# Performance work log

Hardware: AMD Instinct MI355X
Metric: run time of the kernel (lower is better)

The kernel has to match this reference:

```python
import jax, jax.numpy as jnp
import numpy as np

B, S, E, H = 2, 2048, 1024, 16
HD = E // H
SCALE = 1.0 / np.sqrt(HD)
PR_QKV = 0.05   # precision_ratio for q/k/v (critical_attention=False)
PR_OUT = 0.10
ROUTE_THR = 0.05  # gradient_threshold (critical_attention=False)
LN_EPS = 1e-5


def rpb_linear(x, W, b, precision_ratio):
    """ResidualPrecisionBoostLinear: ternary-quantized weight (threshold 0.7*mean|W|,
    per-tensor scale) plus top-`precision_ratio` fraction of residual kept full precision."""
    absW = jnp.abs(W)
    thr = 0.7 * jnp.mean(absW)
    tmask = (absW > thr).astype(W.dtype)
    scale = jnp.sum(absW * tmask) / jnp.maximum(jnp.sum(tmask), 1.0)
    Wq = scale * jnp.sign(W) * tmask
    res = W - Wq
    k = int(precision_ratio * W.size)
    kth = jax.lax.top_k(jnp.abs(res).ravel(), k)[0][-1]
    W_eff = Wq + res * (jnp.abs(res) >= kth).astype(W.dtype)
    return x @ W_eff.T + b


def selective_route(x, threshold):
    # forward: zero out small-magnitude activations (straight-through in training)
    return x * (jnp.abs(x) >= threshold).astype(x.dtype)


def layer_norm(x, g, b):
    mu = jnp.mean(x, axis=-1, keepdims=True)
    var = jnp.mean(jnp.square(x - mu), axis=-1, keepdims=True)
    return (x - mu) * jax.lax.rsqrt(var + LN_EPS) * g + b


def setup_inputs() -> dict:
    key = jax.random.key(0)
    ks = jax.random.split(key, 12)
    f = lambda k, shp, s=1.0: jax.random.normal(k, shp, dtype=jnp.float32) * s
    return {
        "query": f(ks[0], (B, S, E)),
        "key": f(ks[1], (B, S, E)),
        "value": f(ks[2], (B, S, E)),
        "Wq": f(ks[3], (E, E), 0.02), "bq": jnp.zeros((E,), jnp.float32),
        "Wk": f(ks[4], (E, E), 0.02), "bk": jnp.zeros((E,), jnp.float32),
        "Wv": f(ks[5], (E, E), 0.02), "bv": jnp.zeros((E,), jnp.float32),
        "Wo": f(ks[6], (E, E), 0.02), "bo": jnp.zeros((E,), jnp.float32),
        "ln_g": jnp.ones((E,), jnp.float32),
        "ln_b": jnp.zeros((E,), jnp.float32),
    }


def reference(query, key, value, Wq, bq, Wk, bk, Wv, bv, Wo, bo, ln_g, ln_b):
    qn = layer_norm(query, ln_g, ln_b)
    q = selective_route(rpb_linear(qn, Wq, bq, PR_QKV), ROUTE_THR)
    k = selective_route(rpb_linear(key, Wk, bk, PR_QKV), ROUTE_THR)
    v = selective_route(rpb_linear(value, Wv, bv, PR_QKV), ROUTE_THR)
    # [B,S,E] -> [B,H,S,HD]
    q = q.reshape(B, S, H, HD).transpose(0, 2, 1, 3)
    k = k.reshape(B, S, H, HD).transpose(0, 2, 1, 3)
    v = v.reshape(B, S, H, HD).transpose(0, 2, 1, 3)
    scores = jnp.einsum("bhqd,bhkd->bhqk", q, k) * SCALE
    attn = jax.nn.softmax(scores, axis=-1)   # dropout is identity in eval
    ctx = jnp.einsum("bhqk,bhkd->bhqd", attn, v)
    ctx = ctx.transpose(0, 2, 1, 3).reshape(B, S, E)
    return rpb_linear(ctx, Wo, bo, PR_OUT)
```

## Files before the change

### kernel.cpp

```cpp
#include <hip/hip_runtime.h>
#include <stdio.h>
#include <stdint.h>

#define BB 2
#define SS 2048
#define ED 1024
#define HH 16
#define HDD 64
#define MROWS 4096
#define NW_ELEM 1048576u

typedef unsigned short ushortT;
typedef __attribute__((ext_vector_type(8))) short bf16x8;
typedef __attribute__((ext_vector_type(4))) float f32x4;
typedef __attribute__((ext_vector_type(16))) float f32x16;

#define U_WHI 0u
#define U_WLO 4194304u
#define U_XQ  8388608u
#define U_XK  12582912u
#define U_XV  16777216u
#define U_QH  20971520u
#define U_KH  25165824u
#define U_VH  29360128u
#define LP_OFF  33554432u
#define P0_OFF  67108864u
#define P1_OFF  83886080u
#define SMALL_OFF  100663296u
#define HIST_OFF   SMALL_OFF
#define ABS_OFF    (SMALL_OFF + 16384u)
#define MSK_OFF    (ABS_OFF + 32u)
#define CNT_OFF    (MSK_OFF + 32u)
#define SMALL_BYTES 16464u
#define WS_NEEDED  (SMALL_OFF + SMALL_BYTES)

#define SC44 17592186044416.0f
#define INV44 (1.0 / 17592186044416.0)
#define QSCALE 0.18033688011112042f

__device__ __forceinline__ const float* wsel(int w, const float* W0, const float* W1,
                                             const float* W2, const float* W3) {
  return w == 0 ? W0 : w == 1 ? W1 : w == 2 ? W2 : W3;
}

__device__ __forceinline__ ushortT f2bf(float x) {
  unsigned u = __float_as_uint(x);
  unsigned r = (u + 0x7FFFu + ((u >> 16) & 1u)) >> 16;
  return (ushortT)r;
}
__device__ __forceinline__ float bf2f(ushortT b) {
  return __uint_as_float(((unsigned)b) << 16);
}
__device__ __forceinline__ void bsplit(float x, ushortT& h, ushortT& l) {
  ushortT hb = f2bf(x);
  float hf = bf2f(hb);
  h = hb;
  l = f2bf(x - hf);
}
__device__ __forceinline__ unsigned pkbf(float a, float b) {
  unsigned r;
  asm("v_cvt_pk_bf16_f32 %0, %1, %2" : "=v"(r) : "v"(a), "v"(b));
  return r;
}
__device__ __forceinline__ void plswap(unsigned& a, unsigned& b) {
  asm("v_permlane32_swap_b32 %0, %1" : "+v"(a), "+v"(b));
}
__device__ __forceinline__ float fexp2(float x) {
#if __has_builtin(__builtin_amdgcn_exp2f)
  return __builtin_amdgcn_exp2f(x);
#else
  float r;
  asm("v_exp_f32 %0, %1\n\ts_nop 1" : "=v"(r) : "v"(x));
  return r;
#endif
}

__device__ __forceinline__ void gld_lds16(const ushortT* g, ushortT* s) {
  __builtin_amdgcn_global_load_lds((__attribute__((address_space(1))) void*)g,
                                   (__attribute__((address_space(3))) void*)s, 16, 0, 0);
}

template <int N> __device__ __forceinline__ void waitv() {
  if constexpr (N == 0) asm volatile("s_waitcnt vmcnt(0)" ::: "memory");
  else if constexpr (N == 4) asm volatile("s_waitcnt vmcnt(4)" ::: "memory");
  else if constexpr (N == 6) asm volatile("s_waitcnt vmcnt(6)" ::: "memory");
}
__device__ __forceinline__ void pipe_barrier() {
  __builtin_amdgcn_s_barrier();
  __builtin_amdgcn_sched_barrier(0);
}

__device__ __forceinline__ float get_thr(const unsigned long long* sAbs, int w) {
  return 0.7f * (float)((double)sAbs[w] * INV44 / 1048576.0);
}
__device__ __forceinline__ float get_scale(const unsigned long long* sMsk,
                                           const unsigned* cnt, int w) {
  double s = (double)sMsk[w] * INV44;
  return (float)s / fmaxf((float)cnt[w], 1.0f);
}

__device__ __forceinline__ void scan_sel(const unsigned* hist, unsigned& k, unsigned& prefix,
                                         unsigned* sh, int t) {
  sh[t] = hist[t];
  __syncthreads();
  for (int off = 1; off < 256; off <<= 1) {
    unsigned add = (t + off < 256) ? sh[t + off] : 0u;
    __syncthreads();
    sh[t] += add;
    __syncthreads();
  }
  int sel = __syncthreads_count((int)(sh[t] >= k)) - 1;
  unsigned suf = sh[sel];
  k -= (suf - hist[sel]);
  prefix = (prefix << 8) | (unsigned)sel;
  __syncthreads();
}

__global__ __launch_bounds__(256) void k_wstats(const float* W0, const float* W1,
                                                const float* W2, const float* W3,
                                                unsigned long long* sAbs) {
  const int w = blockIdx.y, t = threadIdx.x;
  const float* W = wsel(w, W0, W1, W2, W3) + blockIdx.x * 4096;
  unsigned long long s = 0;
#pragma unroll
  for (int r = 0; r < 4; r++) {
    float4 v = *(const float4*)(W + (t + 256 * r) * 4);
    s += (unsigned long long)(fabsf(v.x) * SC44);
    s += (unsigned long long)(fabsf(v.y) * SC44);
    s += (unsigned long long)(fabsf(v.z) * SC44);
    s += (unsigned long long)(fabsf(v.w) * SC44);
  }
  __shared__ unsigned long long sd[256];
  sd[t] = s;
  __syncthreads();
  for (int off = 128; off > 0; off >>= 1) {
    if (t < off) sd[t] += sd[t + off];
    __syncthreads();
  }
  if (!t) atomicAdd(&sAbs[w], sd[0]);
}

__global__ __launch_bounds__(256) void k_masked(const float* W0, const float* W1,
                                                const float* W2, const float* W3,
                                                const unsigned long long* sAbs,
                                                unsigned long long* sMsk, unsigned* sCnt) {
  const int w = blockIdx.y, t = threadIdx.x;
  const float thr = get_thr(sAbs, w);
  const float* W = wsel(w, W0, W1, W2, W3) + blockIdx.x * 4096;
  unsigned long long s = 0;
  unsigned c = 0;
#pragma unroll
  for (int r = 0; r < 4; r++) {
    float4 v = *(const float4*)(W + (t + 256 * r) * 4);
    float xs[4] = {v.x, v.y, v.z, v.w};
#pragma unroll
    for (int q = 0; q < 4; q++) {
      float a = fabsf(xs[q]);
      if (a > thr) { s += (unsigned long long)(a * SC44); c++; }
    }
  }
  __shared__ unsigned long long sd[256];
  __shared__ unsigned sc[256];
  sd[t] = s; sc[t] = c;
  __syncthreads();
  for (int off = 128; off > 0; off >>= 1) {
    if (t < off) { sd[t] += sd[t + off]; sc[t] += sc[t + off]; }
    __syncthreads();
  }
  if (!t) { atomicAdd(&sMsk[w], sd[0]); atomicAdd(&sCnt[w], sc[0]); }
}

__global__ __launch_bounds__(256) void k_hist(const float* W0, const float* W1,
                                              const float* W2, const float* W3,
                                              const unsigned long long* sAbs,
                                              const unsigned long long* sMsk,
                                              const unsigned* sCnt,
                                              unsigned* histG, int pass) {
  const int w = blockIdx.y, t = threadIdx.x;
  __shared__ unsigned sh[256];
  __shared__ unsigned h[256];
  const float thr = get_thr(sAbs, w);
  const float scale = get_scale(sMsk, sCnt, w);
  unsigned k = (w == 3) ? 104857u : 52428u, prefix = 0u;
  for (int pp = 0; pp < pass; pp++)
    scan_sel(histG + (pp * 4 + w) * 256, k, prefix, sh, t);

  h[t] = 0;
  __syncthreads();
  const float* W = wsel(w, W0, W1, W2, W3) + blockIdx.x * 4096;
  const int shift1 = 32 - 8 * pass;
  const int shift2 = 24 - 8 * pass;
#pragma unroll
  for (int r = 0; r < 4; r++) {
    float4 v = *(const float4*)(W + (t + 256 * r) * 4);
    float xs[4] = {v.x, v.y, v.z, v.w};
#pragma unroll
    for (int q = 0; q < 4; q++) {
      float x = xs[q];
      float a = fabsf(x);
      float wq = (a > thr) ? copysignf(scale, x) : 0.0f;
      unsigned bits = __float_as_uint(fabsf(x - wq));
      if (pass == 0) {
        atomicAdd(&h[bits >> 24], 1u);
      } else {
        if ((bits >> shift1) == prefix)
          atomicAdd(&h[(bits >> shift2) & 255u], 1u);
      }
    }
  }
  __syncthreads();
  if (h[t]) atomicAdd(&histG[(pass * 4 + w) * 256 + t], h[t]);
}

__global__ __launch_bounds__(256) void k_weff(const float* W0, const float* W1,
                                              const float* W2, const float* W3,
                                              const unsigned long long* sAbs,
                                              const unsigned long long* sMsk,
                                              const unsigned* sCnt,
                                              const unsigned* histG,
                                              ushortT* Whi, ushortT* Wlo) {
  const int w = blockIdx.y, t = threadIdx.x;
  __shared__ unsigned sh[256];
  const float thr = get_thr(sAbs, w);
  const float scale = get_scale(sMsk, sCnt, w);
  unsigned k = (w == 3) ? 104857u : 52428u, kth = 0u;
  for (int pp = 0; pp < 4; pp++)
    scan_sel(histG + (pp * 4 + w) * 256, k, kth, sh, t);

  const unsigned idx = (blockIdx.x * 256 + t) * 4;
  const float* W = wsel(w, W0, W1, W2, W3);
  float4 v = *(const float4*)(W + idx);
  float xs[4] = {v.x, v.y, v.z, v.w};
  ushort4 h4, l4;
#pragma unroll
  for (int c = 0; c < 4; c++) {
    float x = xs[c];
    float a = fabsf(x);
    float wq = (a > thr) ? copysignf(scale, x) : 0.0f;
    float res = x - wq;
    unsigned bits = __float_as_uint(fabsf(res));
    float we = wq + ((bits >= kth) ? res : 0.0f);
    ushortT hh, ll;
    bsplit(we, hh, ll);
    ((ushortT*)&h4)[c] = hh;
    ((ushortT*)&l4)[c] = ll;
  }
  *(ushort4*)&Whi[(size_t)w * NW_ELEM + idx] = h4;
  *(ushort4*)&Wlo[(size_t)w * NW_ELEM + idx] = l4;
}

__global__ __launch_bounds__(256) void k_pre(const float* __restrict__ query,
                                             const float* __restrict__ key,
                                             const float* __restrict__ value,
                                             const float* __restrict__ g,
                                             const float* __restrict__ b,
                                             ushortT* __restrict__ Xq,
                                             ushortT* __restrict__ Xk,
                                             ushortT* __restrict__ Xv) {
  const int t = threadIdx.x;
  if (blockIdx.y == 0) {
    const int row = blockIdx.x;
    __shared__ float red[8];
    float4 v = *(const float4*)&query[(size_t)row * ED + t * 4];
    float s = v.x + v.y + v.z + v.w;
#pragma unroll
    for (int m = 32; m; m >>= 1) s += __shfl_xor(s, m, 64);
    if ((t & 63) == 0) red[t >> 6] = s;
    __syncthreads();
    float mu = (red[0] + red[1] + red[2] + red[3]) * (1.0f / 1024.0f);
    float dx = v.x - mu, dy = v.y - mu, dz = v.z - mu, dw = v.w - mu;
    float s2 = dx * dx + dy * dy + dz * dz + dw * dw;
#pragma unroll
    for (int m = 32; m; m >>= 1) s2 += __shfl_xor(s2, m, 64);
    if ((t & 63) == 0) red[4 + (t >> 6)] = s2;
    __syncthreads();
    float var = (red[4] + red[5] + red[6] + red[7]) * (1.0f / 1024.0f);
    float inv = rsqrtf(var + 1e-5f);
    float4 gg = *(const float4*)&g[t * 4];
    float4 bb = *(const float4*)&b[t * 4];
    float ys[4] = {dx * inv * gg.x + bb.x, dy * inv * gg.y + bb.y,
                   dz * inv * gg.z + bb.z, dw * inv * gg.w + bb.w};
    ushort4 h4;
#pragma unroll
    for (int c = 0; c < 4; c++) ((ushortT*)&h4)[c] = f2bf(ys[c]);
    *(ushort4*)&Xq[(size_t)row * ED + t * 4] = h4;
  } else {
    const float* src = (blockIdx.y == 1) ? key : value;
    ushortT* dst = (blockIdx.y == 1) ? Xk : Xv;
    const int i = (blockIdx.x * 256 + t) * 4;
    float4 v = *(const float4*)&src[i];
    ushort4 h4;
    h4.x = f2bf(v.x); h4.y = f2bf(v.y); h4.z = f2bf(v.z); h4.w = f2bf(v.w);
    *(ushort4*)&dst[i] = h4;
  }
}

__device__ __forceinline__ f32x4 mfma16(bf16x8 a, bf16x8 b, f32x4 c) {
  return __builtin_amdgcn_mfma_f32_16x16x32_bf16(a, b, c, 0, 0, 0);
}

template <int MODE, bool ALO, bool WLO, int BK, int MINW>
__global__ __launch_bounds__(256, MINW) void k_gemmP(
    const ushortT* __restrict__ A0, const ushortT* __restrict__ A0l,
    const ushortT* __restrict__ A1,
    const ushortT* __restrict__ Wh, const ushortT* __restrict__ Wl,
    const float* __restrict__ bias0, const float* __restrict__ bias1,
    ushortT* __restrict__ Cb0, ushortT* __restrict__ Cb1,
    float* __restrict__ Cf) {
  constexpr int ABUF = (BK == 64) ? 8192 : 4096;
  constexpr int BBUF = (BK == 64) ? 4096 : 2048;
  constexpr int L = ((BK == 64) ? 4 : 2) * (1 + (ALO ? 1 : 0)) +
                    ((BK == 64) ? 2 : 1) * (1 + (WLO ? 1 : 0));
  constexpr int NT = 1024 / BK;
  __shared__ __align__(16) ushortT sAh[3 * ABUF];
  __shared__ __align__(16) ushortT sAl[ALO ? 3 * ABUF : 8];
  __shared__ __align__(16) ushortT sBh[3 * BBUF];
  __shared__ __align__(16) ushortT sBl[WLO ? 3 * BBUF : 8];

  const int t = threadIdx.x;
  const int w = t >> 6, l = t & 63;
  const int wr = w >> 1, wc = w & 1;

  const int which = (MODE == 0) ? (blockIdx.x >> 9) : 0;
  const int wid = blockIdx.x & 511;
  int id2 = (wid & 7) * 64 + (wid >> 3);
  const int m0 = (id2 >> 4) * 128, n0 = (id2 & 15) * 64;

  const ushortT* A = (MODE == 0 && which) ? A1 : A0;
  const ushortT* Wha = Wh + (MODE == 0 ? (unsigned)which * NW_ELEM : 0u);
  const float* bias = (MODE == 0 && which) ? bias1 : bias0;

  const int sr = l >> 3, swz = (l & 7) ^ sr;
  const int srow = l >> 2, sgr = (l & 3) ^ ((l >> 3) & 3);

  auto stage = [&](int kt, int buf) {
    if constexpr (BK == 64) {
#pragma unroll
      for (int s2 = 0; s2 < 4; s2++) {
        int seg = w * 4 + s2;
        size_t ga = (size_t)(m0 + seg * 8 + sr) * ED + kt * 64 + swz * 8;
        gld_lds16(A + ga, sAh + buf * ABUF + seg * 512);
        if constexpr (ALO) gld_lds16(A0l + ga, sAl + buf * ABUF + seg * 512);
      }
#pragma unroll
      for (int s2 = 0; s2 < 2; s2++) {
        int seg = w * 2 + s2;
        size_t gb = (size_t)(n0 + seg * 8 + sr) * ED + kt * 64 + swz * 8;
        gld_lds16(Wha + gb, sBh + buf * BBUF + seg * 512);
        if constexpr (WLO) gld_lds16(Wl + gb, sBl + buf * BBUF + seg * 512);
      }
    } else {
#pragma unroll
      for (int s2 = 0; s2 < 2; s2++) {
        int seg = w * 2 + s2;
        size_t ga = (size_t)(m0 + seg * 16 + srow) * ED + kt * 32 + sgr * 8;
        gld_lds16(A + ga, sAh + buf * ABUF + seg * 512);
        if constexpr (ALO) gld_lds16(A0l + ga, sAl + buf * ABUF + seg * 512);
      }
      {
        size_t gb = (size_t)(n0 + w * 16 + srow) * ED + kt * 32 + sgr * 8;
        gld_lds16(Wha + gb, sBh + buf * BBUF + w * 512);
        if constexpr (WLO) gld_lds16(Wl + gb, sBl + buf * BBUF + w * 512);
      }
    }
  };

  f32x4 acc[4][2];
#pragma unroll
  for (int i = 0; i < 4; i++)
#pragma unroll
    for (int j = 0; j < 2; j++) acc[i][j] = (f32x4){0.0f, 0.0f, 0.0f, 0.0f};

  auto compute = [&](int buf) {
    if constexpr (BK == 64) {
#pragma unroll
      for (int ks = 0; ks < 2; ks++) {
        bf16x8 ah[4], al[4], bh2[2], bl2[2];
        const int G = ks * 4 + (l >> 4);
#pragma unroll
        for (int i = 0; i < 4; i++) {
          int r = wr * 64 + i * 16 + (l & 15);
          int off = buf * ABUF + r * 64 + ((G ^ (l & 7)) << 3);
          ah[i] = *(const bf16x8*)&sAh[off];
          if constexpr (ALO) al[i] = *(const bf16x8*)&sAl[off];
        }
#pragma unroll
        for (int j = 0; j < 2; j++) {
          int r = wc * 32 + j * 16 + (l & 15);
          int off = buf * BBUF + r * 64 + ((G ^ (l & 7)) << 3);
          bh2[j] = *(const bf16x8*)&sBh[off];
          if constexpr (WLO) bl2[j] = *(const bf16x8*)&sBl[off];
        }
#pragma unroll
        for (int i = 0; i < 4; i++)
#pragma unroll
          for (int j = 0; j < 2; j++) {
            acc[i][j] = mfma16(ah[i], bh2[j], acc[i][j]);
            if constexpr (WLO) acc[i][j] = mfma16(ah[i], bl2[j], acc[i][j]);
            if constexpr (ALO) acc[i][j] = mfma16(al[i], bh2[j], acc[i][j]);
          }
      }
    } else {
      bf16x8 ah[4], al[4], bh2[2], bl2[2];
      const int G = l >> 4;
#pragma unroll
      for (int i = 0; i < 4; i++) {
        int r = wr * 64 + i * 16 + (l & 15);
        int off = buf * ABUF + r * 32 + ((G ^ ((r >> 1) & 3)) << 3);
        ah[i] = *(const bf16x8*)&sAh[off];
        if constexpr (ALO) al[i] = *(const bf16x8*)&sAl[off];
      }
#pragma unroll
      for (int j = 0; j < 2; j++) {
        int r = wc * 32 + j * 16 + (l & 15);
        int off = buf * BBUF + r * 32 + ((G ^ ((r >> 1) & 3)) << 3);
        bh2[j] = *(const bf16x8*)&sBh[off];
        if constexpr (WLO) bl2[j] = *(const bf16x8*)&sBl[off];
      }
#pragma unroll
      for (int i = 0; i < 4; i++)
#pragma unroll
        for (int j = 0; j < 2; j++) {
          acc[i][j] = mfma16(ah[i], bh2[j], acc[i][j]);
          if constexpr (WLO) acc[i][j] = mfma16(ah[i], bl2[j], acc[i][j]);
          if constexpr (ALO) acc[i][j] = mfma16(al[i], bh2[j], acc[i][j]);
        }
    }
  };

  stage(0, 0);
  stage(1, 1);
  for (int kt = 0; kt < NT; ++kt) {
    if (kt < NT - 1) waitv<L>(); else waitv<0>();
    pipe_barrier();
    if (kt + 2 < NT) stage(kt + 2, (kt + 2) % 3);
    __builtin_amdgcn_s_setprio(1);
    compute(kt % 3);
    __builtin_amdgcn_s_setprio(0);
  }

  const int coln = l & 15, row4 = (l >> 4) * 4;
  float bn[2];
#pragma unroll
  for (int j = 0; j < 2; j++) bn[j] = bias[n0 + wc * 32 + j * 16 + coln];
  const int b_ = m0 >> 11, h_ = n0 >> 6;

  if constexpr (MODE == 1) {
#pragma unroll
    for (int i = 0; i < 4; i++)
#pragma unroll
      for (int j = 0; j < 2; j++) {
        int n = n0 + wc * 32 + j * 16 + coln;
#pragma unroll
        for (int r = 0; r < 4; r++) {
          int m = m0 + wr * 64 + i * 16 + row4 + r;
          Cf[(size_t)m * ED + n] = acc[i][j][r] + bn[j];
        }
      }
  } else if constexpr (MODE == 0) {
    const float osc = (which == 0) ? QSCALE : 1.0f;
    ushortT* C = which ? Cb1 : Cb0;
#pragma unroll
    for (int i = 0; i < 4; i++)
#pragma unroll
      for (int j = 0; j < 2; j++) {
        int hd = wc * 32 + j * 16 + coln;
#pragma unroll
        for (int r = 0; r < 4; r++) {
          int m = m0 + wr * 64 + i * 16 + row4 + r;
          int s_ = m & 2047;
          float y = acc[i][j][r] + bn[j];
          y = (fabsf(y) >= 0.05f) ? y : 0.0f;
          y *= osc;
          C[((size_t)(b_ * HH + h_) * SS + s_) * HDD + hd] = f2bf(y);
        }
      }
  } else {
#pragma unroll
    for (int i = 0; i < 4; i++)
#pragma unroll
      for (int j = 0; j < 2; j++) {
        int hd = wc * 32 + j * 16 + coln;
        int s0_ = (m0 + wr * 64 + i * 16 + row4) & 2047;
        ushort4 h4;
#pragma unroll
        for (int r = 0; r < 4; r++) {
          float y = acc[i][j][r] + bn[j];
          y = (fabsf(y) >= 0.05f) ? y : 0.0f;
          ((ushortT*)&h4)[r] = f2bf(y);
        }
        *(ushort4*)&Cb0[((size_t)(b_ * HH + h_) * HDD + hd) * SS + s0_] = h4;
      }
  }
}

__device__ __forceinline__ f32x16 mfma32(bf16x8 a, bf16x8 b, f32x16 c) {
  return __builtin_amdgcn_mfma_f32_32x32x16_bf16(a, b, c, 0, 0, 0);
}

__device__ __forceinline__ void exppack(const f32x16& A, float* ls4,
                                        bf16x8& paA, bf16x8& paB) {
  float p[16];
#pragma unroll
  for (int r = 0; r < 16; r++) {
    p[r] = fexp2(A[r]);
    ls4[r & 3] += p[r];
  }
  unsigned c0 = pkbf(p[0], p[1]), c1 = pkbf(p[2], p[3]);
  unsigned c2 = pkbf(p[4], p[5]), c3 = pkbf(p[6], p[7]);
  unsigned c4 = pkbf(p[8], p[9]), c5 = pkbf(p[10], p[11]);
  unsigned c6 = pkbf(p[12], p[13]), c7 = pkbf(p[14], p[15]);
  plswap(c0, c2); plswap(c1, c3); plswap(c4, c6); plswap(c5, c7);
  uint4 ta = make_uint4(c0, c1, c2, c3);
  uint4 tb = make_uint4(c4, c5, c6, c7);
  paA = __builtin_bit_cast(bf16x8, ta);
  paB = __builtin_bit_cast(bf16x8, tb);
}

__global__ __launch_bounds__(256, 4) void k_attn(
    const ushortT* __restrict__ Qh, const ushortT* __restrict__ Kh,
    const ushortT* __restrict__ Vh,
    float* __restrict__ Pp, float* __restrict__ Lp) {
  __shared__ __align__(16) ushortT sK[2 * 4096];
  __shared__ __align__(16) ushortT sV[2 * 4096];

  const int t = threadIdx.x;
  const int w = t >> 6, l = t & 63;
  const int l32 = l & 31, g = l >> 5;

  int id = blockIdx.x;
  int id2 = (id & 7) * 128 + (id >> 3);
  const int bh = id2 >> 5;
  const int qt = (id2 >> 1) & 15;
  const int half = id2 & 1;

  const size_t kqbase = (size_t)bh * (SS * HDD);
  const size_t vbase = (size_t)bh * (HDD * SS);
  const int q0 = qt * 128 + w * 32;
  const int sbase = half * 1024;

  bf16x8 qh[4];
  const size_t qrow = kqbase + (size_t)(q0 + l32) * HDD;
#pragma unroll
  for (int ks = 0; ks < 4; ks++) qh[ks] = *(const bf16x8*)&Qh[qrow + ks * 16 + g * 8];

  f32x16 octx0, octx1;
#pragma unroll
  for (int i = 0; i < 16; i++) { octx0[i] = 0.0f; octx1[i] = 0.0f; }
  float ls4[4] = {0.0f, 0.0f, 0.0f, 0.0f};

  const int srow = l >> 3;
  const int sgr = (l & 7) ^ srow;

  auto stageA = [&](int kt, int buf) {
    const int s0 = sbase + kt * 64;
#pragma unroll
    for (int s2 = 0; s2 < 2; s2++) {
      int seg = w * 2 + s2;
      int row = seg * 8 + srow;
      gld_lds16(Kh + kqbase + (size_t)(s0 + row) * HDD + sgr * 8, sK + buf * 4096 + seg * 512);
      gld_lds16(Vh + vbase + (size_t)row * SS + s0 + sgr * 8, sV + buf * 4096 + seg * 512);
    }
  };

  stageA(0, 0);
  __syncthreads();

  for (int kt = 0; kt < 16; ++kt) {
    if (kt < 15) stageA(kt + 1, (kt + 1) & 1);
    const ushortT* cK = sK + (kt & 1) * 4096;
    const ushortT* cV = sV + (kt & 1) * 4096;

    f32x16 acc0, acc1;
#pragma unroll
    for (int i = 0; i < 16; i++) { acc0[i] = 0.0f; acc1[i] = 0.0f; }
#pragma unroll
    for (int ks = 0; ks < 4; ks++) {
      int sw = ((ks * 2 + g) ^ (l32 & 7)) << 3;
      bf16x8 kh0 = *(const bf16x8*)&cK[l32 * 64 + sw];
      bf16x8 kh1 = *(const bf16x8*)&cK[(32 + l32) * 64 + sw];
      acc0 = mfma32(kh0, qh[ks], acc0);
      acc1 = mfma32(kh1, qh[ks], acc1);
    }

    bf16x8 pa0, pa1, pa2, pa3;
    exppack(acc0, ls4, pa0, pa1);
    exppack(acc1, ls4, pa2, pa3);

#pragma unroll
    for (int js = 0; js < 4; js++) {
      bf16x8 pj = js == 0 ? pa0 : js == 1 ? pa1 : js == 2 ? pa2 : pa3;
      int vsw = ((js * 2 + g) ^ (l32 & 7)) << 3;
      bf16x8 vh0 = *(const bf16x8*)&cV[l32 * 64 + vsw];
      bf16x8 vh1 = *(const bf16x8*)&cV[(32 + l32) * 64 + vsw];
      octx0 = mfma32(pj, vh0, octx0);
      octx1 = mfma32(pj, vh1, octx1);
    }
    __syncthreads();
  }

  float lsum = (ls4[0] + ls4[1]) + (ls4[2] + ls4[3]);
  float ls = lsum + __shfl_xor(lsum, 32, 64);
  if (g == 0) Lp[half * 65536 + bh * 2048 + q0 + l32] = ls;

  float* P = Pp + (size_t)half * 4194304u;
#pragma unroll
  for (int r = 0; r < 16; r++) {
    int q = (r & 3) + 8 * (r >> 2) + 4 * g;
    size_t pb = ((size_t)bh * 2048 + q0 + q) * 64;
    P[pb + l32] = octx0[r];
    P[pb + 32 + l32] = octx1[r];
  }
}

__global__ __launch_bounds__(256) void k_reduce(const float* __restrict__ Pp,
                                                const float* __restrict__ Lp,
                                                ushortT* __restrict__ ctxH,
                                                ushortT* __restrict__ ctxL) {
  const unsigned i4 = (blockIdx.x * 256 + threadIdx.x) * 4;
  const int d = i4 & 63;
  const int sq = (i4 >> 6) & 2047;
  const int bh = i4 >> 17;
  float ls = Lp[bh * 2048 + sq] + Lp[65536 + bh * 2048 + sq];
  float inv = 1.0f / ls;
  float4 a = *(const float4*)&Pp[i4];
  float4 b = *(const float4*)&Pp[4194304u + i4];
  float os[4] = {(a.x + b.x) * inv, (a.y + b.y) * inv,
                 (a.z + b.z) * inv, (a.w + b.w) * inv};
  ushort4 h4, l4;
#pragma unroll
  for (int c = 0; c < 4; c++) {
    ushortT hh, ll;
    bsplit(os[c], hh, ll);
    ((ushortT*)&h4)[c] = hh;
    ((ushortT*)&l4)[c] = ll;
  }
  size_t ci = ((size_t)((bh >> 4) * 2048 + sq)) * 1024 + (bh & 15) * 64 + d;
  *(ushort4*)&ctxH[ci] = h4;
  *(ushort4*)&ctxL[ci] = l4;
}

extern "C" void kernel_launch(void* const* d_in, const int* in_sizes, int n_in,
                              void* d_out, int out_size, void* d_ws, size_t ws_size,
                              hipStream_t stream) {
  const float* query = (const float*)d_in[0];
  const float* key   = (const float*)d_in[1];
  const float* value = (const float*)d_in[2];
  const float* Wq = (const float*)d_in[3];
  const float* bq = (const float*)d_in[4];
  const float* Wk = (const float*)d_in[5];
  const float* bk = (const float*)d_in[6];
  const float* Wv = (const float*)d_in[7];
  const float* bv = (const float*)d_in[8];
  const float* Wo = (const float*)d_in[9];
  const float* bo = (const float*)d_in[10];
  const float* lng = (const float*)d_in[11];
  const float* lnb = (const float*)d_in[12];
  float* out = (float*)d_out;

  if (ws_size < (size_t)WS_NEEDED) {
    fprintf(stderr, "kernel_launch: ws too small (%zu < %u)\n", ws_size, WS_NEEDED);
    return;
  }

  ushortT* wsu = (ushortT*)d_ws;
  ushortT* Whi = wsu + U_WHI;
  ushortT* Wlo = wsu + U_WLO;
  ushortT* Xq  = wsu + U_XQ;
  ushortT* Xk  = wsu + U_XK;
  ushortT* Xv  = wsu + U_XV;
  ushortT* Qhp = wsu + U_QH;
  ushortT* Khp = wsu + U_KH;
  ushortT* Vhp = wsu + U_VH;
  ushortT* Chp = wsu + U_XQ;
  ushortT* Clp = wsu + U_XK;

  char* wsb = (char*)d_ws;
  float* Pp = (float*)(wsb + P0_OFF);
  float* Lp = (float*)(wsb + LP_OFF);
  unsigned* histG = (unsigned*)(wsb + HIST_OFF);
  unsigned long long* sAbs = (unsigned long long*)(wsb + ABS_OFF);
  unsigned long long* sMsk = (unsigned long long*)(wsb + MSK_OFF);
  unsigned* sCnt = (unsigned*)(wsb + CNT_OFF);

  hipMemsetAsync(histG, 0, SMALL_BYTES, stream);

  k_pre<<<dim3(MROWS, 3), 256, 0, stream>>>(query, key, value, lng, lnb, Xq, Xk, Xv);

  dim3 gW(256, 4);
  k_wstats<<<gW, 256, 0, stream>>>(Wq, Wk, Wv, Wo, sAbs);
  k_masked<<<gW, 256, 0, stream>>>(Wq, Wk, Wv, Wo, sAbs, sMsk, sCnt);
  for (int pass = 0; pass < 4; ++pass)
    k_hist<<<gW, 256, 0, stream>>>(Wq, Wk, Wv, Wo, sAbs, sMsk, sCnt, histG, pass);
  k_weff<<<dim3(1024, 4), 256, 0, stream>>>(Wq, Wk, Wv, Wo, sAbs, sMsk, sCnt, histG,
                                            Whi, Wlo);

  k_gemmP<0, false, false, 64, 2><<<1024, 256, 0, stream>>>(
      Xq, nullptr, Xk, Whi, nullptr, bq, bk, Qhp, Khp, nullptr);
  k_gemmP<2, false, true, 32, 3><<<512, 256, 0, stream>>>(
      Xv, nullptr, nullptr, Whi + 2 * NW_ELEM, Wlo + 2 * NW_ELEM, bv, nullptr,
      Vhp, nullptr, nullptr);

  k_attn<<<1024, 256, 0, stream>>>(Qhp, Khp, Vhp, Pp, Lp);
  k_reduce<<<4096, 256, 0, stream>>>(Pp, Lp, Chp, Clp);

  k_gemmP<1, true, true, 32, 2><<<512, 256, 0, stream>>>(
      Chp, Clp, nullptr, Whi + 3 * NW_ELEM, Wlo + 3 * NW_ELEM, bo, nullptr,
      nullptr, nullptr, out);
}
```

Before: 241.7 us.

## Fuse preprocessing and weight-quantization kernels into one cooperative persistent kernel

Replaces the memset, the LN/cast kernel, and the eight weight-statistics, histogram-radix-select and W_eff kernels with a single cooperative launch of 512 blocks. Grid-wide syncs separate the phases, and the histogram and counter zeroing moves inside the kernel. This removes per-launch overhead and launch gaps across roughly ten small kernels. In exchange, the fixed 512-block grid may underuse bandwidth in the streaming phases, the grid syncs add cost, and the old launch sequence is kept as a fallback if the cooperative launch fails.

```diff
diff --git a/kernel.cpp b/kernel.cpp
--- a/kernel.cpp
+++ b/kernel.cpp
@@ -1,6 +1,9 @@
 #include <hip/hip_runtime.h>
+#include <hip/hip_cooperative_groups.h>
 #include <stdio.h>
 #include <stdint.h>
+
+namespace cg = cooperative_groups;
 
 #define BB 2
 #define SS 2048
@@ -116,6 +119,203 @@
   __syncthreads();
 }
 
+__device__ __forceinline__ void ln_unit(const float* __restrict__ query,
+                                        const float* __restrict__ g,
+                                        const float* __restrict__ b,
+                                        ushortT* __restrict__ Xq,
+                                        int row, int t, float* red) {
+  float4 v = *(const float4*)&query[(size_t)row * ED + t * 4];
+  float s = v.x + v.y + v.z + v.w;
+#pragma unroll
+  for (int m = 32; m; m >>= 1) s += __shfl_xor(s, m, 64);
+  if ((t & 63) == 0) red[t >> 6] = s;
+  __syncthreads();
+  float mu = (red[0] + red[1] + red[2] + red[3]) * (1.0f / 1024.0f);
+  float dx = v.x - mu, dy = v.y - mu, dz = v.z - mu, dw = v.w - mu;
+  float s2 = dx * dx + dy * dy + dz * dz + dw * dw;
+#pragma unroll
+  for (int m = 32; m; m >>= 1) s2 += __shfl_xor(s2, m, 64);
+  if ((t & 63) == 0) red[4 + (t >> 6)] = s2;
+  __syncthreads();
+  float var = (red[4] + red[5] + red[6] + red[7]) * (1.0f / 1024.0f);
+  float inv = rsqrtf(var + 1e-5f);
+  float4 gg = *(const float4*)&g[t * 4];
+  float4 bb = *(const float4*)&b[t * 4];
+  float ys[4] = {dx * inv * gg.x + bb.x, dy * inv * gg.y + bb.y,
+                 dz * inv * gg.z + bb.z, dw * inv * gg.w + bb.w};
+  ushort4 h4;
+#pragma unroll
+  for (int c = 0; c < 4; c++) ((ushortT*)&h4)[c] = f2bf(ys[c]);
+  *(ushort4*)&Xq[(size_t)row * ED + t * 4] = h4;
+}
+
+__device__ __forceinline__ void cast_unit(const float* __restrict__ src,
+                                          ushortT* __restrict__ dst, int idx, int t) {
+  const int i = (idx * 256 + t) * 4;
+  float4 v = *(const float4*)&src[i];
+  ushort4 h4;
+  h4.x = f2bf(v.x); h4.y = f2bf(v.y); h4.z = f2bf(v.z); h4.w = f2bf(v.w);
+  *(ushort4*)&dst[i] = h4;
+}
+
+__global__ __launch_bounds__(256, 2) void k_prep(
+    const float* W0, const float* W1, const float* W2, const float* W3,
+    const float* query, const float* key, const float* value,
+    const float* g, const float* b,
+    ushortT* Xq, ushortT* Xk, ushortT* Xv,
+    unsigned long long* sAbs, unsigned long long* sMsk, unsigned* sCnt,
+    unsigned* histG, ushortT* Whi, ushortT* Wlo) {
+  const int t = threadIdx.x, bid = blockIdx.x;
+  cg::grid_group grid = cg::this_grid();
+  __shared__ unsigned sh[256];
+  __shared__ unsigned hloc[256];
+  __shared__ float red[8];
+  __shared__ unsigned long long sdU[256];
+  __shared__ unsigned scU[256];
+
+  if (bid < 16) histG[bid * 256 + t] = 0;
+  if (bid == 16 && t < 4) { sAbs[t] = 0; sMsk[t] = 0; sCnt[t] = 0; }
+#pragma unroll 1
+  for (int u0 = 0; u0 < 24; ++u0) {
+    const int u = bid * 24 + u0;
+    const int type = u >> 12, idx = u & 4095;
+    if (type == 0) ln_unit(query, g, b, Xq, idx, t, red);
+    else if (type == 1) cast_unit(key, Xk, idx, t);
+    else cast_unit(value, Xv, idx, t);
+  }
+  __threadfence();
+  grid.sync();
+
+#pragma unroll 1
+  for (int ci = 0; ci < 2; ++ci) {
+    const int c = bid * 2 + ci, w = c >> 8;
+    const float* W = wsel(w, W0, W1, W2, W3) + (c & 255) * 4096;
+    unsigned long long s = 0;
+#pragma unroll
+    for (int r = 0; r < 4; r++) {
+      float4 v = *(const float4*)(W + (t + 256 * r) * 4);
+      s += (unsigned long long)(fabsf(v.x) * SC44);
+      s += (unsigned long long)(fabsf(v.y) * SC44);
+      s += (unsigned long long)(fabsf(v.z) * SC44);
+      s += (unsigned long long)(fabsf(v.w) * SC44);
+    }
+    sdU[t] = s;
+    __syncthreads();
+    for (int off = 128; off > 0; off >>= 1) {
+      if (t < off) sdU[t] += sdU[t + off];
+      __syncthreads();
+    }
+    if (!t) atomicAdd(&sAbs[w], sdU[0]);
+    __syncthreads();
+  }
+  __threadfence();
+  grid.sync();
+
+#pragma unroll 1
+  for (int ci = 0; ci < 2; ++ci) {
+    const int c = bid * 2 + ci, w = c >> 8;
+    const float thr = get_thr(sAbs, w);
+    const float* W = wsel(w, W0, W1, W2, W3) + (c & 255) * 4096;
+    unsigned long long s = 0;
+    unsigned cc = 0;
+#pragma unroll
+    for (int r = 0; r < 4; r++) {
+      float4 v = *(const float4*)(W + (t + 256 * r) * 4);
+      float xs[4] = {v.x, v.y, v.z, v.w};
+#pragma unroll
+      for (int q = 0; q < 4; q++) {
+        float a = fabsf(xs[q]);
+        if (a > thr) { s += (unsigned long long)(a * SC44); cc++; }
+      }
+    }
+    sdU[t] = s; scU[t] = cc;
+    __syncthreads();
+    for (int off = 128; off > 0; off >>= 1) {
+      if (t < off) { sdU[t] += sdU[t + off]; scU[t] += scU[t + off]; }
+      __syncthreads();
+    }
+    if (!t) { atomicAdd(&sMsk[w], sdU[0]); atomicAdd(&sCnt[w], scU[0]); }
+    __syncthreads();
+  }
+  __threadfence();
+  grid.sync();
+
+#pragma unroll 1
+  for (int p = 0; p < 4; ++p) {
+    const int shift1 = 32 - 8 * p;
+    const int shift2 = 24 - 8 * p;
+#pragma unroll 1
+    for (int ci = 0; ci < 2; ++ci) {
+      const int c = bid * 2 + ci, w = c >> 8;
+      const float thr = get_thr(sAbs, w);
+      const float scale = get_scale(sMsk, sCnt, w);
+      unsigned k = (w == 3) ? 104857u : 52428u, prefix = 0u;
+      for (int pp = 0; pp < p; pp++)
+        scan_sel(histG + (pp * 4 + w) * 256, k, prefix, sh, t);
+      hloc[t] = 0;
+      __syncthreads();
+      const float* W = wsel(w, W0, W1, W2, W3) + (c & 255) * 4096;
+#pragma unroll
+      for (int r = 0; r < 4; r++) {
+        float4 v = *(const float4*)(W + (t + 256 * r) * 4);
+        float xs[4] = {v.x, v.y, v.z, v.w};
+#pragma unroll
+        for (int q = 0; q < 4; q++) {
+          float x = xs[q];
+          float a = fabsf(x);
+          float wq = (a > thr) ? copysignf(scale, x) : 0.0f;
+          unsigned bits = __float_as_uint(fabsf(x - wq));
+          if (p == 0) {
+            atomicAdd(&hloc[bits >> 24], 1u);
+          } else {
+            if ((bits >> shift1) == prefix)
+              atomicAdd(&hloc[(bits >> shift2) & 255u], 1u);
+          }
+        }
+      }
+      __syncthreads();
+      if (hloc[t]) atomicAdd(&histG[(p * 4 + w) * 256 + t], hloc[t]);
+      __syncthreads();
+    }
+    __threadfence();
+    grid.sync();
+  }
+
+#pragma unroll 1
+  for (int ci = 0; ci < 2; ++ci) {
+    const int c = bid * 2 + ci, w = c >> 8;
+    const float thr = get_thr(sAbs, w);
+    const float scale = get_scale(sMsk, sCnt, w);
+    unsigned k = (w == 3) ? 104857u : 52428u, kth = 0u;
+    for (int pp = 0; pp < 4; pp++)
+      scan_sel(histG + (pp * 4 + w) * 256, k, kth, sh, t);
+    const float* W = wsel(w, W0, W1, W2, W3) + (c & 255) * 4096;
+    const size_t obase = (size_t)w * NW_ELEM + (unsigned)(c & 255) * 4096u;
+#pragma unroll
+    for (int r = 0; r < 4; r++) {
+      const int e0 = (t + 256 * r) * 4;
+      float4 v = *(const float4*)(W + e0);
+      float xs[4] = {v.x, v.y, v.z, v.w};
+      ushort4 h4, l4;
+#pragma unroll
+      for (int cq = 0; cq < 4; cq++) {
+        float x = xs[cq];
+        float a = fabsf(x);
+        float wq = (a > thr) ? copysignf(scale, x) : 0.0f;
+        float res = x - wq;
+        unsigned bits = __float_as_uint(fabsf(res));
+        float we = wq + ((bits >= kth) ? res : 0.0f);
+        ushortT hh, ll;
+        bsplit(we, hh, ll);
+        ((ushortT*)&h4)[cq] = hh;
+        ((ushortT*)&l4)[cq] = ll;
+      }
+      *(ushort4*)&Whi[obase + e0] = h4;
+      *(ushort4*)&Wlo[obase + e0] = l4;
+    }
+  }
+}
+
 __global__ __launch_bounds__(256) void k_wstats(const float* W0, const float* W1,
                                                 const float* W2, const float* W3,
                                                 unsigned long long* sAbs) {
@@ -258,41 +458,10 @@
                                              ushortT* __restrict__ Xk,
                                              ushortT* __restrict__ Xv) {
   const int t = threadIdx.x;
-  if (blockIdx.y == 0) {
-    const int row = blockIdx.x;
-    __shared__ float red[8];
-    float4 v = *(const float4*)&query[(size_t)row * ED + t * 4];
-    float s = v.x + v.y + v.z + v.w;
-#pragma unroll
-    for (int m = 32; m; m >>= 1) s += __shfl_xor(s, m, 64);
-    if ((t & 63) == 0) red[t >> 6] = s;
-    __syncthreads();
-    float mu = (red[0] + red[1] + red[2] + red[3]) * (1.0f / 1024.0f);
-    float dx = v.x - mu, dy = v.y - mu, dz = v.z - mu, dw = v.w - mu;
-    float s2 = dx * dx + dy * dy + dz * dz + dw * dw;
-#pragma unroll
-    for (int m = 32; m; m >>= 1) s2 += __shfl_xor(s2, m, 64);
-    if ((t & 63) == 0) red[4 + (t >> 6)] = s2;
-    __syncthreads();
-    float var = (red[4] + red[5] + red[6] + red[7]) * (1.0f / 1024.0f);
-    float inv = rsqrtf(var + 1e-5f);
-    float4 gg = *(const float4*)&g[t * 4];
-    float4 bb = *(const float4*)&b[t * 4];
-    float ys[4] = {dx * inv * gg.x + bb.x, dy * inv * gg.y + bb.y,
-                   dz * inv * gg.z + bb.z, dw * inv * gg.w + bb.w};
-    ushort4 h4;
-#pragma unroll
-    for (int c = 0; c < 4; c++) ((ushortT*)&h4)[c] = f2bf(ys[c]);
-    *(ushort4*)&Xq[(size_t)row * ED + t * 4] = h4;
-  } else {
-    const float* src = (blockIdx.y == 1) ? key : value;
-    ushortT* dst = (blockIdx.y == 1) ? Xk : Xv;
-    const int i = (blockIdx.x * 256 + t) * 4;
-    float4 v = *(const float4*)&src[i];
-    ushort4 h4;
-    h4.x = f2bf(v.x); h4.y = f2bf(v.y); h4.z = f2bf(v.z); h4.w = f2bf(v.w);
-    *(ushort4*)&dst[i] = h4;
-  }
+  __shared__ float red[8];
+  if (blockIdx.y == 0) ln_unit(query, g, b, Xq, blockIdx.x, t, red);
+  else if (blockIdx.y == 1) cast_unit(key, Xk, blockIdx.x, t);
+  else cast_unit(value, Xv, blockIdx.x, t);
 }
 
 __device__ __forceinline__ f32x4 mfma16(bf16x8 a, bf16x8 b, f32x4 c) {
@@ -683,17 +852,25 @@
   unsigned long long* sMsk = (unsigned long long*)(wsb + MSK_OFF);
   unsigned* sCnt = (unsigned*)(wsb + CNT_OFF);
 
-  hipMemsetAsync(histG, 0, SMALL_BYTES, stream);
-
-  k_pre<<<dim3(MROWS, 3), 256, 0, stream>>>(query, key, value, lng, lnb, Xq, Xk, Xv);
-
-  dim3 gW(256, 4);
-  k_wstats<<<gW, 256, 0, stream>>>(Wq, Wk, Wv, Wo, sAbs);
-  k_masked<<<gW, 256, 0, stream>>>(Wq, Wk, Wv, Wo, sAbs, sMsk, sCnt);
-  for (int pass = 0; pass < 4; ++pass)
-    k_hist<<<gW, 256, 0, stream>>>(Wq, Wk, Wv, Wo, sAbs, sMsk, sCnt, histG, pass);
-  k_weff<<<dim3(1024, 4), 256, 0, stream>>>(Wq, Wk, Wv, Wo, sAbs, sMsk, sCnt, histG,
-                                            Whi, Wlo);
+  void* args[] = {(void*)&Wq, (void*)&Wk, (void*)&Wv, (void*)&Wo,
+                  (void*)&query, (void*)&key, (void*)&value,
+                  (void*)&lng, (void*)&lnb,
+                  (void*)&Xq, (void*)&Xk, (void*)&Xv,
+                  (void*)&sAbs, (void*)&sMsk, (void*)&sCnt,
+                  (void*)&histG, (void*)&Whi, (void*)&Wlo};
+  hipError_t ce = hipLaunchCooperativeKernel((const void*)k_prep, dim3(512),
+                                             dim3(256), args, 0, stream);
+  if (ce != hipSuccess) {
+    hipMemsetAsync(histG, 0, SMALL_BYTES, stream);
+    k_pre<<<dim3(MROWS, 3), 256, 0, stream>>>(query, key, value, lng, lnb, Xq, Xk, Xv);
+    dim3 gW(256, 4);
+    k_wstats<<<gW, 256, 0, stream>>>(Wq, Wk, Wv, Wo, sAbs);
+    k_masked<<<gW, 256, 0, stream>>>(Wq, Wk, Wv, Wo, sAbs, sMsk, sCnt);
+    for (int pass = 0; pass < 4; ++pass)
+      k_hist<<<gW, 256, 0, stream>>>(Wq, Wk, Wv, Wo, sAbs, sMsk, sCnt, histG, pass);
+    k_weff<<<dim3(1024, 4), 256, 0, stream>>>(Wq, Wk, Wv, Wo, sAbs, sMsk, sCnt, histG,
+                                              Whi, Wlo);
+  }
 
   k_gemmP<0, false, false, 64, 2><<<1024, 256, 0, stream>>>(
       Xq, nullptr, Xk, Whi, nullptr, bq, bk, Qhp, Khp, nullptr);
```

New measurement: 899.5 us. +272.2%, slower.

## Fuse weight stats into pre kernel and split-KV reduce into attention tail

Applied to the files above, without the earlier changes.

Merges the k_wstats weight-abs-sum pass into k_pre as extra blocks, removing one launch. It also removes the separate k_reduce kernel: each attention block bumps a per-tile atomic counter, and the second of the two split-KV blocks to finish combines the partial outputs and normalisers and writes the bf16 hi/lo context. The aim is to save launch overhead and let the reduce overlap with other attention blocks. The cost is a threadfence plus atomic per block and a serial tail inside the last block of each tile, and correctness depends on the tile counters being zeroed by the memset.

```diff
diff --git a/kernel.cpp b/kernel.cpp
--- a/kernel.cpp
+++ b/kernel.cpp
@@ -31,7 +31,8 @@
 #define ABS_OFF    (SMALL_OFF + 16384u)
 #define MSK_OFF    (ABS_OFF + 32u)
 #define CNT_OFF    (MSK_OFF + 32u)
-#define SMALL_BYTES 16464u
+#define TCNT_OFF   (SMALL_OFF + 16464u)
+#define SMALL_BYTES 18512u
 #define WS_NEEDED  (SMALL_OFF + SMALL_BYTES)
 
 #define SC44 17592186044416.0f
@@ -116,28 +117,85 @@
   __syncthreads();
 }
 
-__global__ __launch_bounds__(256) void k_wstats(const float* W0, const float* W1,
-                                                const float* W2, const float* W3,
-                                                unsigned long long* sAbs) {
-  const int w = blockIdx.y, t = threadIdx.x;
-  const float* W = wsel(w, W0, W1, W2, W3) + blockIdx.x * 4096;
-  unsigned long long s = 0;
-#pragma unroll
-  for (int r = 0; r < 4; r++) {
-    float4 v = *(const float4*)(W + (t + 256 * r) * 4);
-    s += (unsigned long long)(fabsf(v.x) * SC44);
-    s += (unsigned long long)(fabsf(v.y) * SC44);
-    s += (unsigned long long)(fabsf(v.z) * SC44);
-    s += (unsigned long long)(fabsf(v.w) * SC44);
-  }
+__device__ __forceinline__ void ln_unit(const float* __restrict__ query,
+                                        const float* __restrict__ g,
+                                        const float* __restrict__ b,
+                                        ushortT* __restrict__ Xq,
+                                        int row, int t, float* red) {
+  float4 v = *(const float4*)&query[(size_t)row * ED + t * 4];
+  float s = v.x + v.y + v.z + v.w;
+#pragma unroll
+  for (int m = 32; m; m >>= 1) s += __shfl_xor(s, m, 64);
+  if ((t & 63) == 0) red[t >> 6] = s;
+  __syncthreads();
+  float mu = (red[0] + red[1] + red[2] + red[3]) * (1.0f / 1024.0f);
+  float dx = v.x - mu, dy = v.y - mu, dz = v.z - mu, dw = v.w - mu;
+  float s2 = dx * dx + dy * dy + dz * dz + dw * dw;
+#pragma unroll
+  for (int m = 32; m; m >>= 1) s2 += __shfl_xor(s2, m, 64);
+  if ((t & 63) == 0) red[4 + (t >> 6)] = s2;
+  __syncthreads();
+  float var = (red[4] + red[5] + red[6] + red[7]) * (1.0f / 1024.0f);
+  float inv = rsqrtf(var + 1e-5f);
+  float4 gg = *(const float4*)&g[t * 4];
+  float4 bb = *(const float4*)&b[t * 4];
+  float ys[4] = {dx * inv * gg.x + bb.x, dy * inv * gg.y + bb.y,
+                 dz * inv * gg.z + bb.z, dw * inv * gg.w + bb.w};
+  ushort4 h4;
+#pragma unroll
+  for (int c = 0; c < 4; c++) ((ushortT*)&h4)[c] = f2bf(ys[c]);
+  *(ushort4*)&Xq[(size_t)row * ED + t * 4] = h4;
+}
+
+__device__ __forceinline__ void cast_unit(const float* __restrict__ src,
+                                          ushortT* __restrict__ dst, int idx, int t) {
+  const int i = (idx * 256 + t) * 4;
+  float4 v = *(const float4*)&src[i];
+  ushort4 h4;
+  h4.x = f2bf(v.x); h4.y = f2bf(v.y); h4.z = f2bf(v.z); h4.w = f2bf(v.w);
+  *(ushort4*)&dst[i] = h4;
+}
+
+__global__ __launch_bounds__(256) void k_pre(const float* __restrict__ query,
+                                             const float* __restrict__ key,
+                                             const float* __restrict__ value,
+                                             const float* __restrict__ g,
+                                             const float* __restrict__ b,
+                                             const float* W0, const float* W1,
+                                             const float* W2, const float* W3,
+                                             ushortT* __restrict__ Xq,
+                                             ushortT* __restrict__ Xk,
+                                             ushortT* __restrict__ Xv,
+                                             unsigned long long* sAbs) {
+  const int t = threadIdx.x, bid = blockIdx.x;
+  __shared__ float red[8];
   __shared__ unsigned long long sd[256];
-  sd[t] = s;
-  __syncthreads();
-  for (int off = 128; off > 0; off >>= 1) {
-    if (t < off) sd[t] += sd[t + off];
+  if (bid < 4096) {
+    ln_unit(query, g, b, Xq, bid, t, red);
+  } else if (bid < 8192) {
+    cast_unit(key, Xk, bid - 4096, t);
+  } else if (bid < 12288) {
+    cast_unit(value, Xv, bid - 8192, t);
+  } else {
+    const int c = bid - 12288, w = c >> 8;
+    const float* W = wsel(w, W0, W1, W2, W3) + (c & 255) * 4096;
+    unsigned long long s = 0;
+#pragma unroll
+    for (int r = 0; r < 4; r++) {
+      float4 v = *(const float4*)(W + (t + 256 * r) * 4);
+      s += (unsigned long long)(fabsf(v.x) * SC44);
+      s += (unsigned long long)(fabsf(v.y) * SC44);
+      s += (unsigned long long)(fabsf(v.z) * SC44);
+      s += (unsigned long long)(fabsf(v.w) * SC44);
+    }
+    sd[t] = s;
     __syncthreads();
-  }
-  if (!t) atomicAdd(&sAbs[w], sd[0]);
+    for (int off = 128; off > 0; off >>= 1) {
+      if (t < off) sd[t] += sd[t + off];
+      __syncthreads();
+    }
+    if (!t) atomicAdd(&sAbs[w], sd[0]);
+  }
 }
 
 __global__ __launch_bounds__(256) void k_masked(const float* W0, const float* W1,
@@ -247,52 +305,6 @@
   }
   *(ushort4*)&Whi[(size_t)w * NW_ELEM + idx] = h4;
   *(ushort4*)&Wlo[(size_t)w * NW_ELEM + idx] = l4;
-}
-
-__global__ __launch_bounds__(256) void k_pre(const float* __restrict__ query,
-                                             const float* __restrict__ key,
-                                             const float* __restrict__ value,
-                                             const float* __restrict__ g,
-                                             const float* __restrict__ b,
-                                             ushortT* __restrict__ Xq,
-                                             ushortT* __restrict__ Xk,
-                                             ushortT* __restrict__ Xv) {
-  const int t = threadIdx.x;
-  if (blockIdx.y == 0) {
-    const int row = blockIdx.x;
-    __shared__ float red[8];
-    float4 v = *(const float4*)&query[(size_t)row * ED + t * 4];
-    float s = v.x + v.y + v.z + v.w;
-#pragma unroll
-    for (int m = 32; m; m >>= 1) s += __shfl_xor(s, m, 64);
-    if ((t & 63) == 0) red[t >> 6] = s;
-    __syncthreads();
-    float mu = (red[0] + red[1] + red[2] + red[3]) * (1.0f / 1024.0f);
-    float dx = v.x - mu, dy = v.y - mu, dz = v.z - mu, dw = v.w - mu;
-    float s2 = dx * dx + dy * dy + dz * dz + dw * dw;
-#pragma unroll
-    for (int m = 32; m; m >>= 1) s2 += __shfl_xor(s2, m, 64);
-    if ((t & 63) == 0) red[4 + (t >> 6)] = s2;
-    __syncthreads();
-    float var = (red[4] + red[5] + red[6] + red[7]) * (1.0f / 1024.0f);
-    float inv = rsqrtf(var + 1e-5f);
-    float4 gg = *(const float4*)&g[t * 4];
-    float4 bb = *(const float4*)&b[t * 4];
-    float ys[4] = {dx * inv * gg.x + bb.x, dy * inv * gg.y + bb.y,
-                   dz * inv * gg.z + bb.z, dw * inv * gg.w + bb.w};
-    ushort4 h4;
-#pragma unroll
-    for (int c = 0; c < 4; c++) ((ushortT*)&h4)[c] = f2bf(ys[c]);
-    *(ushort4*)&Xq[(size_t)row * ED + t * 4] = h4;
-  } else {
-    const float* src = (blockIdx.y == 1) ? key : value;
-    ushortT* dst = (blockIdx.y == 1) ? Xk : Xv;
-    const int i = (blockIdx.x * 256 + t) * 4;
-    float4 v = *(const float4*)&src[i];
-    ushort4 h4;
-    h4.x = f2bf(v.x); h4.y = f2bf(v.y); h4.z = f2bf(v.z); h4.w = f2bf(v.w);
-    *(ushort4*)&dst[i] = h4;
-  }
 }
 
 __device__ __forceinline__ f32x4 mfma16(bf16x8 a, bf16x8 b, f32x4 c) {
@@ -520,9 +532,12 @@
 __global__ __launch_bounds__(256, 4) void k_attn(
     const ushortT* __restrict__ Qh, const ushortT* __restrict__ Kh,
     const ushortT* __restrict__ Vh,
-    float* __restrict__ Pp, float* __restrict__ Lp) {
+    float* __restrict__ Pp, float* __restrict__ Lp,
+    ushortT* __restrict__ ctxH, ushortT* __restrict__ ctxL,
+    unsigned* __restrict__ tileCnt) {
   __shared__ __align__(16) ushortT sK[2 * 4096];
   __shared__ __align__(16) ushortT sV[2 * 4096];
+  __shared__ unsigned oldc;
 
   const int t = threadIdx.x;
   const int w = t >> 6, l = t & 63;
@@ -611,33 +626,39 @@
     P[pb + l32] = octx0[r];
     P[pb + 32 + l32] = octx1[r];
   }
-}
-
-__global__ __launch_bounds__(256) void k_reduce(const float* __restrict__ Pp,
-                                                const float* __restrict__ Lp,
-                                                ushortT* __restrict__ ctxH,
-                                                ushortT* __restrict__ ctxL) {
-  const unsigned i4 = (blockIdx.x * 256 + threadIdx.x) * 4;
-  const int d = i4 & 63;
-  const int sq = (i4 >> 6) & 2047;
-  const int bh = i4 >> 17;
-  float ls = Lp[bh * 2048 + sq] + Lp[65536 + bh * 2048 + sq];
-  float inv = 1.0f / ls;
-  float4 a = *(const float4*)&Pp[i4];
-  float4 b = *(const float4*)&Pp[4194304u + i4];
-  float os[4] = {(a.x + b.x) * inv, (a.y + b.y) * inv,
-                 (a.z + b.z) * inv, (a.w + b.w) * inv};
-  ushort4 h4, l4;
-#pragma unroll
-  for (int c = 0; c < 4; c++) {
-    ushortT hh, ll;
-    bsplit(os[c], hh, ll);
-    ((ushortT*)&h4)[c] = hh;
-    ((ushortT*)&l4)[c] = ll;
-  }
-  size_t ci = ((size_t)((bh >> 4) * 2048 + sq)) * 1024 + (bh & 15) * 64 + d;
-  *(ushort4*)&ctxH[ci] = h4;
-  *(ushort4*)&ctxL[ci] = l4;
+
+  const int tile = bh * 16 + qt;
+  __threadfence();
+  if (t == 0) oldc = atomicAdd(&tileCnt[tile], 1u);
+  __syncthreads();
+  if (oldc == 1) {
+    __threadfence();
+    const int b_ = bh >> 4, h_ = bh & 15;
+#pragma unroll 1
+    for (int u = 0; u < 8; ++u) {
+      const int e4 = (u * 256 + t) * 4;
+      const int sq = qt * 128 + (e4 >> 6);
+      const int d = e4 & 63;
+      const unsigned gi = ((unsigned)bh * 2048u + (unsigned)sq) * 64u + d;
+      float lsv = Lp[bh * 2048 + sq] + Lp[65536 + bh * 2048 + sq];
+      float inv = 1.0f / lsv;
+      float4 a = *(const float4*)&Pp[gi];
+      float4 b4 = *(const float4*)&Pp[4194304u + gi];
+      float os[4] = {(a.x + b4.x) * inv, (a.y + b4.y) * inv,
+                     (a.z + b4.z) * inv, (a.w + b4.w) * inv};
+      ushort4 h4, l4;
+#pragma unroll
+      for (int cq = 0; cq < 4; cq++) {
+        ushortT hh, ll;
+        bsplit(os[cq], hh, ll);
+        ((ushortT*)&h4)[cq] = hh;
+        ((ushortT*)&l4)[cq] = ll;
+      }
+      size_t ci = ((size_t)(b_ * SS + sq)) * 1024 + h_ * 64 + d;
+      *(ushort4*)&ctxH[ci] = h4;
+      *(ushort4*)&ctxL[ci] = l4;
+    }
+  }
 }
 
 extern "C" void kernel_launch(void* const* d_in, const int* in_sizes, int n_in,
@@ -682,13 +703,14 @@
   unsigned long long* sAbs = (unsigned long long*)(wsb + ABS_OFF);
   unsigned long long* sMsk = (unsigned long long*)(wsb + MSK_OFF);
   unsigned* sCnt = (unsigned*)(wsb + CNT_OFF);
+  unsigned* tileCnt = (unsigned*)(wsb + TCNT_OFF);
 
   hipMemsetAsync(histG, 0, SMALL_BYTES, stream);
 
-  k_pre<<<dim3(MROWS, 3), 256, 0, stream>>>(query, key, value, lng, lnb, Xq, Xk, Xv);
+  k_pre<<<13312, 256, 0, stream>>>(query, key, value, lng, lnb,
+                                   Wq, Wk, Wv, Wo, Xq, Xk, Xv, sAbs);
 
   dim3 gW(256, 4);
-  k_wstats<<<gW, 256, 0, stream>>>(Wq, Wk, Wv, Wo, sAbs);
   k_masked<<<gW, 256, 0, stream>>>(Wq, Wk, Wv, Wo, sAbs, sMsk, sCnt);
   for (int pass = 0; pass < 4; ++pass)
     k_hist<<<gW, 256, 0, stream>>>(Wq, Wk, Wv, Wo, sAbs, sMsk, sCnt, histG, pass);
@@ -701,8 +723,7 @@
       Xv, nullptr, nullptr, Whi + 2 * NW_ELEM, Wlo + 2 * NW_ELEM, bv, nullptr,
       Vhp, nullptr, nullptr);
 
-  k_attn<<<1024, 256, 0, stream>>>(Qhp, Khp, Vhp, Pp, Lp);
-  k_reduce<<<4096, 256, 0, stream>>>(Pp, Lp, Chp, Clp);
+  k_attn<<<1024, 256, 0, stream>>>(Qhp, Khp, Vhp, Pp, Lp, Chp, Clp, tileCnt);
 
   k_gemmP<1, true, true, 32, 2><<<512, 256, 0, stream>>>(
       Chp, Clp, nullptr, Whi + 3 * NW_ELEM, Wlo + 3 * NW_ELEM, bo, nullptr,
```

Result: slower. 414.4 us (+71.5%).
